# Optimization experiments

Hardware: AMD Instinct MI355X
Metric: run time of the kernel (lower is better)

Reference implementation:

```python
import jax, jax.numpy as jnp
import numpy as np

C0 = 16          # embed channels (c0) == mamba d_model
OUT_DIM = 32
D_INNER = 32     # expand * c0
D_STATE = 16
D_CONV = 4
DT_RANK = 1      # max(1, d_model // 16)
EPS = 1e-5


def setup_inputs():
    key = jax.random.key(0)
    ks = jax.random.split(key, 32)

    def n(i, shape, s):
        return (jax.random.normal(ks[i], shape) * s).astype(jnp.float32)

    inp = {
        "x": jax.random.normal(ks[0], (1, 4, 64, 64, 64), jnp.float32),
        "embed_w": n(1, (4, C0, 1, 7, 7, 7), 0.1),   # 4 per-modality conv7 stems
        "ln_g": jnp.ones((C0,), jnp.float32),
        "ln_b": jnp.zeros((C0,), jnp.float32),
        "in_proj_w": n(2, (2 * D_INNER, C0), 0.25),
        "out_proj_w": n(3, (C0, D_INNER), 0.18),
        "up_w": n(4, (C0, OUT_DIM, 2, 2, 2), 0.2),   # ConvTranspose3d k=2 s=2
    }
    for j, sfx in enumerate(["", "_b"]):             # forward / backward scan params
        b = 5 + 7 * j
        inp["conv_w" + sfx] = n(b, (D_INNER, 1, D_CONV), 0.3)
        inp["conv_b" + sfx] = n(b + 1, (D_INNER,), 0.1)
        inp["xproj_w" + sfx] = n(b + 2, (DT_RANK + 2 * D_STATE, D_INNER), 0.15)
        inp["dtproj_w" + sfx] = n(b + 3, (D_INNER, DT_RANK), 0.5)
        inp["dtproj_b" + sfx] = jnp.full((D_INNER,), -4.6, jnp.float32)  # softplus ~= 0.01
        inp["A_log" + sfx] = jnp.log(jnp.tile(jnp.arange(1, D_STATE + 1, dtype=jnp.float32), (D_INNER, 1)))
        inp["D_skip" + sfx] = jnp.ones((D_INNER,), jnp.float32)
    return inp


def _instnorm(x):
    m = jnp.mean(x, axis=(2, 3, 4), keepdims=True)
    v = jnp.mean(jnp.square(x - m), axis=(2, 3, 4), keepdims=True)
    return (x - m) / jnp.sqrt(v + EPS)


def _embed(x1, w):
    # Conv3d(1, c0, k=7, s=2, p=3, bias=False) -> InstanceNorm3d -> GELU(exact)
    y = jax.lax.conv_general_dilated(x1, w, (2, 2, 2), [(3, 3)] * 3,
                                     dimension_numbers=('NCDHW', 'OIDHW', 'NCDHW'))
    return jax.nn.gelu(_instnorm(y), approximate=False)


def _branch(u, z, cw, cb, xw, dtw, dtb, A_log, D_skip):
    # One Mamba scan branch. u, z: [B, L, Dn]
    Dn = u.shape[-1]
    uc = jax.lax.conv_general_dilated(jnp.swapaxes(u, 1, 2), cw, (1,), [(D_CONV - 1, 0)],
                                      feature_group_count=Dn,
                                      dimension_numbers=('NCH', 'OIH', 'NCH'))
    u = jax.nn.silu(jnp.swapaxes(uc + cb[None, :, None], 1, 2))       # causal dw-conv + SiLU
    xdbl = u @ xw.T                                                   # [B,L,R+2N]
    dt = jax.nn.softplus(xdbl[..., :DT_RANK] @ dtw.T + dtb)           # [B,L,Dn]
    Bm = xdbl[..., DT_RANK:DT_RANK + D_STATE]                         # [B,L,N]
    Cm = xdbl[..., DT_RANK + D_STATE:]                                # [B,L,N]
    A = -jnp.exp(A_log)                                               # [Dn,N]
    a = jnp.exp(dt[..., None] * A)                                    # [B,L,Dn,N]
    b = (dt * u)[..., None] * Bm[:, :, None, :]                       # [B,L,Dn,N]

    def comb(c1, c2):
        a1, b1 = c1
        a2, b2 = c2
        return a1 * a2, a2 * b1 + b2

    _, h = jax.lax.associative_scan(comb, (a, b), axis=1)             # h_t = a_t h_{t-1} + b_t
    y = jnp.einsum('bldn,bln->bld', h, Cm) + u * D_skip
    return y * jax.nn.silu(z)


def _bimamba(t, p):
    xz = t @ p['in_proj_w'].T
    xi, z = jnp.split(xz, 2, axis=-1)
    yf = _branch(xi, z, p['conv_w'], p['conv_b'], p['xproj_w'], p['dtproj_w'],
                 p['dtproj_b'], p['A_log'], p['D_skip'])
    yb = _branch(xi[:, ::-1], z[:, ::-1], p['conv_w_b'], p['conv_b_b'], p['xproj_w_b'],
                 p['dtproj_w_b'], p['dtproj_b_b'], p['A_log_b'], p['D_skip_b'])[:, ::-1]
    return (yf + yb) @ p['out_proj_w'].T


def _mamba_dir(x5, p):
    B, C = x5.shape[:2]
    t = jnp.swapaxes(x5.reshape(B, C, -1), 1, 2)                      # [B, L, C]
    mu = jnp.mean(t, axis=-1, keepdims=True)
    var = jnp.mean(jnp.square(t - mu), axis=-1, keepdims=True)
    t = (t - mu) / jnp.sqrt(var + EPS) * p['ln_g'] + p['ln_b']        # LayerNorm
    t = _bimamba(t, p)
    return jnp.swapaxes(t, 1, 2).reshape(x5.shape)


def _mamba_layer(x5, p):
    # tri-directional scans: (d,w,h), (w,d,h), (h,w,d) + residual
    o1 = _mamba_dir(x5, p)
    o2 = jnp.transpose(_mamba_dir(jnp.transpose(x5, (0, 1, 3, 2, 4)), p), (0, 1, 3, 2, 4))
    o3 = jnp.transpose(_mamba_dir(jnp.transpose(x5, (0, 1, 4, 3, 2)), p), (0, 1, 4, 3, 2))
    return o1 + o2 + o3 + x5


def reference(x, embed_w, ln_g, ln_b, in_proj_w, out_proj_w, up_w,
              conv_w, conv_b, xproj_w, dtproj_w, dtproj_b, A_log, D_skip,
              conv_w_b, conv_b_b, xproj_w_b, dtproj_w_b, dtproj_b_b, A_log_b, D_skip_b):
    p = dict(ln_g=ln_g, ln_b=ln_b, in_proj_w=in_proj_w, out_proj_w=out_proj_w,
             conv_w=conv_w, conv_b=conv_b, xproj_w=xproj_w, dtproj_w=dtproj_w,
             dtproj_b=dtproj_b, A_log=A_log, D_skip=D_skip,
             conv_w_b=conv_w_b, conv_b_b=conv_b_b, xproj_w_b=xproj_w_b,
             dtproj_w_b=dtproj_w_b, dtproj_b_b=dtproj_b_b, A_log_b=A_log_b,
             D_skip_b=D_skip_b)
    us = [_embed(x[:, m:m + 1], embed_w[m]) for m in range(4)]        # 4 modalities
    outs = [_mamba_layer(u, p) for u in us]
    y = outs[0] + outs[1] + outs[2] + outs[3] + us[0] + us[1] + us[2] + us[3]
    B, _, D, H, W = y.shape
    # ConvTranspose3d(c0, out_dim, k=2, s=2): each output 2x2x2 block from one input voxel
    y = jnp.einsum('bcdhw,coijk->bodihjwk', y, up_w).reshape(B, OUT_DIM, 2 * D, 2 * H, 2 * W)
    return y
```

## Files before the change

kernel.cpp:

```cpp
#include <hip/hip_runtime.h>
#include <math.h>

#define L 32768
#define CH 64
#define NC 512

#if __has_builtin(__builtin_amdgcn_exp2f)
#define EXP2(x) __builtin_amdgcn_exp2f(x)
#else
#define EXP2(x) exp2f(x)
#endif

__device__ __forceinline__ int sigma_map(int l, int perm) {
    int b2 = l >> 10, b1 = (l >> 5) & 31, b0 = l & 31;
    if (perm == 0) return (b2 << 10) | (b1 << 5) | b0;
    if (perm == 1) return (b1 << 10) | (b2 << 5) | b0;
    return (b0 << 10) | (b1 << 5) | b2;
}

__device__ __forceinline__ float silu_f(float v) {
    return v / (1.f + __expf(-v));
}
__device__ __forceinline__ float softplus_f(float x) {
    return fmaxf(x, 0.f) + log1pf(__expf(-fabsf(x)));
}

__device__ __forceinline__ float quad_sum(float x) {
    int v = __builtin_amdgcn_update_dpp(0, __float_as_int(x), 0xB1, 0xf, 0xf, true);
    x += __int_as_float(v);
    v = __builtin_amdgcn_update_dpp(0, __float_as_int(x), 0x4E, 0xf, 0xf, true);
    x += __int_as_float(v);
    return x;
}

__global__ __launch_bounds__(256) void k_embed(const float* __restrict__ x,
                                               const float* __restrict__ w,
                                               float* __restrict__ us) {
    __shared__ float tile[10143];
    int bx = blockIdx.x, m = blockIdx.y;
    int c = bx >> 7, sb = bx & 127;
    int zc = sb >> 2, yc0 = (sb & 3) << 3;
    const float* xin = x + m * 262144;
    int iz0 = 2 * zc - 3, iy0 = 2 * yc0 - 3;
    for (int i = threadIdx.x; i < 10143; i += 256) {
        int tz = i / 1449, r = i - tz * 1449;
        int ty = r / 69, tx = r - ty * 69;
        int gz = iz0 + tz, gy = iy0 + ty, gx = tx - 3;
        float v = 0.f;
        if ((unsigned)gz < 64u && (unsigned)gy < 64u && (unsigned)gx < 64u)
            v = xin[(gz * 64 + gy) * 64 + gx];
        tile[i] = v;
    }
    __syncthreads();
    const float* wc = w + (m * 16 + c) * 343;
    int tyl = threadIdx.x >> 5, xc = threadIdx.x & 31;
    float acc = 0.f;
    for (int kz = 0; kz < 7; ++kz)
        for (int ky = 0; ky < 7; ++ky) {
            const float* row = &tile[(kz * 21 + 2 * tyl + ky) * 69 + 2 * xc];
            const float* wr = &wc[kz * 49 + ky * 7];
            #pragma unroll
            for (int kx = 0; kx < 7; ++kx) acc += row[kx] * wr[kx];
        }
    us[(m * 16 + c) * 32768 + sb * 256 + threadIdx.x] = acc;
}

__global__ void k_instnorm_gelu(float* __restrict__ us) {
    int ch = blockIdx.x;
    float* p = us + ch * 32768;
    float s = 0.f, s2 = 0.f;
    for (int i = threadIdx.x; i < 32768; i += 256) { float v = p[i]; s += v; s2 += v * v; }
    __shared__ float rs[256], rs2[256];
    rs[threadIdx.x] = s; rs2[threadIdx.x] = s2;
    __syncthreads();
    for (int o = 128; o > 0; o >>= 1) {
        if (threadIdx.x < o) { rs[threadIdx.x] += rs[threadIdx.x + o]; rs2[threadIdx.x] += rs2[threadIdx.x + o]; }
        __syncthreads();
    }
    float mu = rs[0] * (1.f / 32768.f);
    float var = rs2[0] * (1.f / 32768.f) - mu * mu;
    float rinv = rsqrtf(var + 1e-5f);
    for (int i = threadIdx.x; i < 32768; i += 256) {
        float v = (p[i] - mu) * rinv;
        p[i] = 0.5f * v * (1.f + erff(v * 0.70710678118654752f));
    }
}

__global__ void k_transpose(const float* __restrict__ us, float* __restrict__ us_t) {
    __shared__ float tl[16][257];
    int m = blockIdx.x >> 7, t0 = (blockIdx.x & 127) << 8;
    for (int i = threadIdx.x; i < 4096; i += 256) {
        int c = i >> 8, j = i & 255;
        tl[c][j] = us[(m * 16 + c) * 32768 + t0 + j];
    }
    __syncthreads();
    for (int i = threadIdx.x; i < 4096; i += 256) {
        int j = i >> 4, c = i & 15;
        us_t[(m * 32768 + t0 + j) * 16 + c] = tl[c][j];
    }
}

__global__ __launch_bounds__(512) void k_chunkA(
    const float* __restrict__ us_t, const float* __restrict__ ln_g, const float* __restrict__ ln_b,
    const float* __restrict__ Wip,
    const float* __restrict__ cwA, const float* __restrict__ cbA, const float* __restrict__ xwA,
    const float* __restrict__ dtwA, const float* __restrict__ dtbA, const float* __restrict__ AlA,
    const float* __restrict__ cwB, const float* __restrict__ cbB, const float* __restrict__ xwB,
    const float* __restrict__ dtwB, const float* __restrict__ dtbB, const float* __restrict__ AlB,
    float2* __restrict__ hlPa) {
    __shared__ float sm[8000];
    float* xiT = sm;
    float* uSh = sm + 2304;
    float* sBs = sm + 4480;
    float* xd0 = sm + 5760;
    float* G   = sm + 5824;

    int c = blockIdx.x, dir = blockIdx.y;
    int m = dir / 3, perm = dir - m * 3;
    int p0 = c * CH;
    int tid = threadIdx.x;

    G[tid] = Wip[tid];
    if (tid < 16) G[512 + tid] = ln_g[tid];
    else if (tid < 32) G[512 + tid] = ln_b[tid - 16];
    __syncthreads();

    if (tid < 70) {
        int p = p0 - 3 + tid;
        if ((unsigned)p < (unsigned)L) {
            int sp = sigma_map(p, perm);
            const float4* rw = (const float4*)(us_t + (m * 32768 + sp) * 16);
            float t[16];
            ((float4*)t)[0] = rw[0]; ((float4*)t)[1] = rw[1];
            ((float4*)t)[2] = rw[2]; ((float4*)t)[3] = rw[3];
            float mu = 0.f;
            #pragma unroll
            for (int ci = 0; ci < 16; ++ci) mu += t[ci];
            mu *= (1.f / 16.f);
            float var = 0.f;
            #pragma unroll
            for (int ci = 0; ci < 16; ++ci) { float d = t[ci] - mu; var += d * d; }
            var *= (1.f / 16.f);
            float rinv = rsqrtf(var + 1e-5f);
            #pragma unroll
            for (int ci = 0; ci < 16; ++ci)
                uSh[ci * 72 + tid] = (t[ci] - mu) * rinv * G[512 + ci] + G[528 + ci];
        } else {
            #pragma unroll
            for (int ci = 0; ci < 16; ++ci) uSh[ci * 72 + tid] = 0.f;
        }
    }
    __syncthreads();

    for (int it = tid; it < 576; it += 512) {
        int d = it / 18, q = it - d * 18;
        float ax = 0.f, ay = 0.f, az = 0.f, aw = 0.f;
        #pragma unroll
        for (int ci = 0; ci < 16; ++ci) {
            float4 tq = *(const float4*)&uSh[ci * 72 + 4 * q];
            float wv = G[d * 16 + ci];
            ax += tq.x * wv; ay += tq.y * wv; az += tq.z * wv; aw += tq.w * wv;
        }
        float4 o4 = {ax, ay, az, aw};
        *(float4*)&xiT[d * 72 + 4 * q] = o4;
    }
    __syncthreads();

    for (int b = 0; b < 2; ++b) {
        const float* cw  = b ? cwB  : cwA;
        const float* cb  = b ? cbB  : cbA;
        const float* xw  = b ? xwB  : xwA;
        const float* dtw = b ? dtwB : dtwA;
        const float* dtb = b ? dtbB : dtbA;
        const float* Al  = b ? AlB  : AlA;
        for (int i = tid; i < 544; i += 512) G[i] = xw[i];
        if (tid < 128) G[544 + tid] = cw[tid];
        else if (tid < 160) G[544 + tid] = cb[tid - 128];
        __syncthreads();

        {
            int d = tid >> 4, q = tid & 15, s0 = 4 * q;
            float xr[7];
            if (b == 0) {
                #pragma unroll
                for (int j = 0; j < 7; ++j) xr[j] = xiT[d * 72 + s0 + j];
            } else {
                #pragma unroll
                for (int j = 0; j < 7; ++j) xr[j] = xiT[d * 72 + 63 - s0 + j];
            }
            float w0 = G[544 + d * 4], w1 = G[545 + d * 4], w2 = G[546 + d * 4], w3 = G[547 + d * 4];
            float bias = G[672 + d];
            #pragma unroll
            for (int i = 0; i < 4; ++i) {
                float a;
                if (b == 0) a = bias + xr[i] * w0 + xr[i + 1] * w1 + xr[i + 2] * w2 + xr[i + 3] * w3;
                else        a = bias + xr[6 - i] * w0 + xr[5 - i] * w1 + xr[4 - i] * w2 + xr[3 - i] * w3;
                uSh[d * 68 + s0 + i] = silu_f(a);
            }
        }
        __syncthreads();

        for (int it = tid; it < 272; it += 512) {
            int j = it >> 4, q = it & 15, s0 = 4 * q;
            float ax = 0.f, ay = 0.f, az = 0.f, aw = 0.f;
            #pragma unroll
            for (int ci = 0; ci < 32; ++ci) {
                float4 uq = *(const float4*)&uSh[ci * 68 + s0];
                float wv = G[j * 32 + ci];
                ax += uq.x * wv; ay += uq.y * wv; az += uq.z * wv; aw += uq.w * wv;
            }
            if (j == 0) {
                float4 o4 = {ax, ay, az, aw};
                *(float4*)&xd0[s0] = o4;
            } else {
                sBs[(s0 + 0) * 20 + (j - 1)] = ax;
                sBs[(s0 + 1) * 20 + (j - 1)] = ay;
                sBs[(s0 + 2) * 20 + (j - 1)] = az;
                sBs[(s0 + 3) * 20 + (j - 1)] = aw;
            }
        }
        __syncthreads();

        for (int i = tid; i < 2048; i += 512) {
            int d2 = i >> 6, s = i & 63;
            G[d2 * 68 + s] = softplus_f(xd0[s] * dtw[d2] + dtb[d2]);
        }
        __syncthreads();

        if (tid < 128) {
            int d = tid >> 2, nb = (tid & 3) * 4;
            float kk0 = -1.44269504f * __expf(Al[d * 16 + nb + 0]);
            float kk1 = -1.44269504f * __expf(Al[d * 16 + nb + 1]);
            float kk2 = -1.44269504f * __expf(Al[d * 16 + nb + 2]);
            float kk3 = -1.44269504f * __expf(Al[d * 16 + nb + 3]);
            float h0 = 0.f, h1 = 0.f, h2 = 0.f, h3 = 0.f, sumdt = 0.f;
            const float* dtp = &G[d * 68];
            const float* up  = &uSh[d * 68];
            for (int s0 = 0; s0 < CH; s0 += 4) {
                float4 dt4 = *(const float4*)&dtp[s0];
                float4 u4  = *(const float4*)&up[s0];
                #define ASTEP(DT, UU, SS) { \
                    float w_ = (DT) * (UU); \
                    float4 B4 = *(const float4*)&sBs[(SS) * 20 + nb]; \
                    h0 = fmaf(EXP2((DT) * kk0), h0, w_ * B4.x); \
                    h1 = fmaf(EXP2((DT) * kk1), h1, w_ * B4.y); \
                    h2 = fmaf(EXP2((DT) * kk2), h2, w_ * B4.z); \
                    h3 = fmaf(EXP2((DT) * kk3), h3, w_ * B4.w); \
                    sumdt += (DT); }
                ASTEP(dt4.x, u4.x, s0 + 0)
                ASTEP(dt4.y, u4.y, s0 + 1)
                ASTEP(dt4.z, u4.z, s0 + 2)
                ASTEP(dt4.w, u4.w, s0 + 3)
                #undef ASTEP
            }
            int chunk = b ? (NC - 1 - c) : c;
            float4* o4 = (float4*)(hlPa + (((size_t)(dir * 2 + b) * NC + chunk) * 512) + d * 16 + nb);
            float4 a0 = {h0, EXP2(sumdt * kk0), h1, EXP2(sumdt * kk1)};
            float4 a1 = {h2, EXP2(sumdt * kk2), h3, EXP2(sumdt * kk3)};
            o4[0] = a0; o4[1] = a1;
        }
        __syncthreads();
    }
}

__global__ __launch_bounds__(512) void k_scanB(float2* __restrict__ hlPa) {
    int db = blockIdx.x;
    int t = threadIdx.x;
    float2* base = hlPa + (size_t)db * NC * 512 + t;
    float H = 0.f;
    for (int c0 = 0; c0 < NC; c0 += 8) {
        float2 v[8];
        #pragma unroll
        for (int j = 0; j < 8; ++j) v[j] = base[(c0 + j) * 512];
        #pragma unroll
        for (int j = 0; j < 8; ++j) {
            *((float*)(base + (c0 + j) * 512)) = H;
            H = fmaf(v[j].y, H, v[j].x);
        }
    }
}

__global__ __launch_bounds__(512) void k_chunkC(
    const float* __restrict__ us_t, const float* __restrict__ ln_g, const float* __restrict__ ln_b,
    const float* __restrict__ Wip, const float* __restrict__ Wout,
    const float* __restrict__ cwA, const float* __restrict__ cbA, const float* __restrict__ xwA,
    const float* __restrict__ dtwA, const float* __restrict__ dtbA, const float* __restrict__ AlA,
    const float* __restrict__ DsA,
    const float* __restrict__ cwB, const float* __restrict__ cbB, const float* __restrict__ xwB,
    const float* __restrict__ dtwB, const float* __restrict__ dtbB, const float* __restrict__ AlB,
    const float* __restrict__ DsB,
    const float2* __restrict__ hlPa, float* __restrict__ O) {
    __shared__ float sm[13504];
    float* xiT = sm;
    float* zT  = sm + 2304;
    float* syT = sm + 4608;
    float* uSh = sm + 6784;
    float* sBs = sm + 8960;
    float* sCs = sm + 10240;
    float* xd0 = sm + 11264;
    float* G   = sm + 11328;

    int c = blockIdx.x, dir = blockIdx.y;
    int m = dir / 3, perm = dir - m * 3;
    int p0 = c * CH;
    int tid = threadIdx.x;

    for (int i = tid; i < 1024; i += 512) G[i] = Wip[i];
    if (tid < 16) G[1024 + tid] = ln_g[tid];
    else if (tid < 32) G[1024 + tid] = ln_b[tid - 16];
    __syncthreads();

    if (tid < 70) {
        int p = p0 - 3 + tid;
        if ((unsigned)p < (unsigned)L) {
            int sp = sigma_map(p, perm);
            const float4* rw = (const float4*)(us_t + (m * 32768 + sp) * 16);
            float t[16];
            ((float4*)t)[0] = rw[0]; ((float4*)t)[1] = rw[1];
            ((float4*)t)[2] = rw[2]; ((float4*)t)[3] = rw[3];
            float mu = 0.f;
            #pragma unroll
            for (int ci = 0; ci < 16; ++ci) mu += t[ci];
            mu *= (1.f / 16.f);
            float var = 0.f;
            #pragma unroll
            for (int ci = 0; ci < 16; ++ci) { float d = t[ci] - mu; var += d * d; }
            var *= (1.f / 16.f);
            float rinv = rsqrtf(var + 1e-5f);
            #pragma unroll
            for (int ci = 0; ci < 16; ++ci)
                uSh[ci * 72 + tid] = (t[ci] - mu) * rinv * G[1024 + ci] + G[1040 + ci];
        } else {
            #pragma unroll
            for (int ci = 0; ci < 16; ++ci) uSh[ci * 72 + tid] = 0.f;
        }
    }
    __syncthreads();

    for (int it = tid; it < 1152; it += 512) {
        int dd = it / 18, q = it - dd * 18;
        float ax = 0.f, ay = 0.f, az = 0.f, aw = 0.f;
        #pragma unroll
        for (int ci = 0; ci < 16; ++ci) {
            float4 tq = *(const float4*)&uSh[ci * 72 + 4 * q];
            float wv = G[dd * 16 + ci];
            ax += tq.x * wv; ay += tq.y * wv; az += tq.z * wv; aw += tq.w * wv;
        }
        float4 o4 = {ax, ay, az, aw};
        int d = dd & 31;
        if (dd < 32) *(float4*)&xiT[d * 72 + 4 * q] = o4;
        else         *(float4*)&zT[d * 72 + 4 * q] = o4;
    }
    __syncthreads();

    for (int b = 0; b < 2; ++b) {
        const float* cw  = b ? cwB  : cwA;
        const float* cb  = b ? cbB  : cbA;
        const float* xw  = b ? xwB  : xwA;
        const float* dtw = b ? dtwB : dtwA;
        const float* dtb = b ? dtbB : dtbA;
        const float* Al  = b ? AlB  : AlA;
        const float* Ds  = b ? DsB  : DsA;
        for (int i = tid; i < 1056; i += 512) G[i] = xw[i];
        if (tid < 128) G[1056 + tid] = cw[tid];
        else if (tid < 160) G[1056 + tid] = cb[tid - 128];
        __syncthreads();

        {
            int d = tid >> 4, q = tid & 15, s0 = 4 * q;
            float xr[7];
            if (b == 0) {
                #pragma unroll
                for (int j = 0; j < 7; ++j) xr[j] = xiT[d * 72 + s0 + j];
            } else {
                #pragma unroll
                for (int j = 0; j < 7; ++j) xr[j] = xiT[d * 72 + 63 - s0 + j];
            }
            float w0 = G[1056 + d * 4], w1 = G[1057 + d * 4], w2 = G[1058 + d * 4], w3 = G[1059 + d * 4];
            float bias = G[1184 + d];
            #pragma unroll
            for (int i = 0; i < 4; ++i) {
                float a;
                if (b == 0) a = bias + xr[i] * w0 + xr[i + 1] * w1 + xr[i + 2] * w2 + xr[i + 3] * w3;
                else        a = bias + xr[6 - i] * w0 + xr[5 - i] * w1 + xr[4 - i] * w2 + xr[3 - i] * w3;
                uSh[d * 68 + s0 + i] = silu_f(a);
            }
        }
        __syncthreads();

        for (int it = tid; it < 528; it += 512) {
            int j = it >> 4, q = it & 15, s0 = 4 * q;
            float ax = 0.f, ay = 0.f, az = 0.f, aw = 0.f;
            #pragma unroll
            for (int ci = 0; ci < 32; ++ci) {
                float4 uq = *(const float4*)&uSh[ci * 68 + s0];
                float wv = G[j * 32 + ci];
                ax += uq.x * wv; ay += uq.y * wv; az += uq.z * wv; aw += uq.w * wv;
            }
            if (j == 0) {
                float4 o4 = {ax, ay, az, aw};
                *(float4*)&xd0[s0] = o4;
            } else if (j < 17) {
                sBs[(s0 + 0) * 20 + (j - 1)] = ax;
                sBs[(s0 + 1) * 20 + (j - 1)] = ay;
                sBs[(s0 + 2) * 20 + (j - 1)] = az;
                sBs[(s0 + 3) * 20 + (j - 1)] = aw;
            } else {
                sCs[(s0 + 0) * 16 + (j - 17)] = ax;
                sCs[(s0 + 1) * 16 + (j - 17)] = ay;
                sCs[(s0 + 2) * 16 + (j - 17)] = az;
                sCs[(s0 + 3) * 16 + (j - 17)] = aw;
            }
        }
        __syncthreads();

        for (int i = tid; i < 2048; i += 512) {
            int d2 = i >> 6, s = i & 63;
            G[d2 * 68 + s] = softplus_f(xd0[s] * dtw[d2] + dtb[d2]);
        }
        __syncthreads();

        for (int it = tid; it < 2048; it += 512) {
            int d = it >> 6, s = it & 63;
            float val = uSh[d * 68 + s] * Ds[d];
            if (b == 0) syT[d * 68 + s] = val;
            else        syT[d * 68 + (63 - s)] += val;
        }
        __syncthreads();

        if (tid < 128) {
            int d = tid >> 2, nb = (tid & 3) * 4;
            float kk0 = -1.44269504f * __expf(Al[d * 16 + nb + 0]);
            float kk1 = -1.44269504f * __expf(Al[d * 16 + nb + 1]);
            float kk2 = -1.44269504f * __expf(Al[d * 16 + nb + 2]);
            float kk3 = -1.44269504f * __expf(Al[d * 16 + nb + 3]);
            int chunk = b ? (NC - 1 - c) : c;
            const float2* hp = hlPa + (((size_t)(dir * 2 + b) * NC + chunk) * 512) + d * 16 + nb;
            float h0 = hp[0].x, h1 = hp[1].x, h2 = hp[2].x, h3 = hp[3].x;
            const float* dtp = &G[d * 68];
            const float* up  = &uSh[d * 68];
            for (int s0 = 0; s0 < CH; s0 += 4) {
                float4 dt4 = *(const float4*)&dtp[s0];
                float4 u4  = *(const float4*)&up[s0];
                float pr0, pr1, pr2, pr3;
                #define CSTEP(DT, UU, SS, PR) { \
                    float w_ = (DT) * (UU); \
                    float4 B4 = *(const float4*)&sBs[(SS) * 20 + nb]; \
                    float4 C4 = *(const float4*)&sCs[(SS) * 16 + nb]; \
                    h0 = fmaf(EXP2((DT) * kk0), h0, w_ * B4.x); \
                    h1 = fmaf(EXP2((DT) * kk1), h1, w_ * B4.y); \
                    h2 = fmaf(EXP2((DT) * kk2), h2, w_ * B4.z); \
                    h3 = fmaf(EXP2((DT) * kk3), h3, w_ * B4.w); \
                    float p_ = h0 * C4.x; \
                    p_ = fmaf(h1, C4.y, p_); \
                    p_ = fmaf(h2, C4.z, p_); \
                    p_ = fmaf(h3, C4.w, p_); \
                    PR = quad_sum(p_); }
                CSTEP(dt4.x, u4.x, s0 + 0, pr0)
                CSTEP(dt4.y, u4.y, s0 + 1, pr1)
                CSTEP(dt4.z, u4.z, s0 + 2, pr2)
                CSTEP(dt4.w, u4.w, s0 + 3, pr3)
                #undef CSTEP
                if ((tid & 3) == 0) {
                    if (b == 0) {
                        float4* dst = (float4*)&syT[d * 68 + s0];
                        float4 o = *dst;
                        o.x += pr0; o.y += pr1; o.z += pr2; o.w += pr3;
                        *dst = o;
                    } else {
                        float4* dst = (float4*)&syT[d * 68 + (60 - s0)];
                        float4 o = *dst;
                        o.x += pr3; o.y += pr2; o.z += pr1; o.w += pr0;
                        *dst = o;
                    }
                }
            }
        }
        __syncthreads();
    }

    for (int it = tid; it < 2048; it += 512) {
        int d = it >> 6, pl = it & 63;
        syT[d * 68 + pl] *= silu_f(zT[d * 72 + pl + 3]);
    }
    __syncthreads();

    if (tid < 512) G[tid] = Wout[tid];
    __syncthreads();
    for (int it = tid; it < 1024; it += 512) {
        int p = it >> 4, cc = it & 15;
        float acc = 0.f;
        #pragma unroll
        for (int d = 0; d < 32; ++d) acc += syT[d * 68 + p] * G[cc * 32 + d];
        O[((size_t)(dir * 32768 + p0 + p)) * 16 + cc] = acc;
    }
}

__global__ void k_accum(const float* __restrict__ us_t, const float* __restrict__ O,
                        float* __restrict__ acc_t) {
    int it = blockIdx.x * 256 + threadIdx.x;
    int sp = it >> 2, q = (it & 3) << 2;
    float ax = 0.f, ay = 0.f, az = 0.f, aw = 0.f;
    #pragma unroll
    for (int mm = 0; mm < 4; ++mm) {
        float4 v = *(const float4*)&us_t[(mm * 32768 + sp) * 16 + q];
        ax += 2.f * v.x; ay += 2.f * v.y; az += 2.f * v.z; aw += 2.f * v.w;
    }
    #pragma unroll
    for (int perm = 0; perm < 3; ++perm) {
        int l = sigma_map(sp, perm);
        #pragma unroll
        for (int mm = 0; mm < 4; ++mm) {
            int dir = mm * 3 + perm;
            float4 v = *(const float4*)&O[(dir * 32768 + l) * 16 + q];
            ax += v.x; ay += v.y; az += v.z; aw += v.w;
        }
    }
    float4 o4 = {ax, ay, az, aw};
    *(float4*)&acc_t[sp * 16 + q] = o4;
}

__global__ void k_up(const float* __restrict__ acc_t, const float* __restrict__ upw,
                     float* __restrict__ out) {
    __shared__ float w[4096];
    for (int i = threadIdx.x; i < 4096; i += 256) w[i] = upw[i];
    __syncthreads();
    int e = blockIdx.x * 256 + threadIdx.x;
    int o = e >> 17;
    int r2 = e & 131071;
    int Dz = r2 >> 11, Hy = (r2 >> 5) & 63, Wp = r2 & 31;
    int sp = ((Dz >> 1) << 10) | ((Hy >> 1) << 5) | Wp;
    int wbase = (((Dz & 1) << 2) | ((Hy & 1) << 1));
    const float* arow = &acc_t[sp * 16];
    float v0 = 0.f, v1 = 0.f;
    #pragma unroll
    for (int c = 0; c < 16; ++c) {
        float a = arow[c];
        const float* wr = &w[(c * 32 + o) * 8 + wbase];
        v0 += a * wr[0];
        v1 += a * wr[1];
    }
    float2 ov; ov.x = v0; ov.y = v1;
    *(float2*)&out[((o * 64 + Dz) * 64 + Hy) * 64 + 2 * Wp] = ov;
}

extern "C" void kernel_launch(void* const* d_in, const int* in_sizes, int n_in,
                              void* d_out, int out_size, void* d_ws, size_t ws_size,
                              hipStream_t stream) {
    (void)in_sizes; (void)n_in; (void)out_size; (void)ws_size;
    const float* x    = (const float*)d_in[0];
    const float* embw = (const float*)d_in[1];
    const float* ln_g = (const float*)d_in[2];
    const float* ln_b = (const float*)d_in[3];
    const float* Wip  = (const float*)d_in[4];
    const float* Wout = (const float*)d_in[5];
    const float* upw  = (const float*)d_in[6];
    const float* cwA  = (const float*)d_in[7];
    const float* cbA  = (const float*)d_in[8];
    const float* xwA  = (const float*)d_in[9];
    const float* dtwA = (const float*)d_in[10];
    const float* dtbA = (const float*)d_in[11];
    const float* AlA  = (const float*)d_in[12];
    const float* DsA  = (const float*)d_in[13];
    const float* cwB  = (const float*)d_in[14];
    const float* cbB  = (const float*)d_in[15];
    const float* xwB  = (const float*)d_in[16];
    const float* dtwB = (const float*)d_in[17];
    const float* dtbB = (const float*)d_in[18];
    const float* AlB  = (const float*)d_in[19];
    const float* DsB  = (const float*)d_in[20];

    float* ws    = (float*)d_ws;
    float*  us    = ws;
    float*  us_t  = ws + 2097152;
    float2* hlPa  = (float2*)(ws + 4194304);
    float*  O     = ws + 16777216;
    float*  acc_t = ws + 23068672;

    k_embed<<<dim3(2048, 4), 256, 0, stream>>>(x, embw, us);
    k_instnorm_gelu<<<64, 256, 0, stream>>>(us);
    k_transpose<<<512, 256, 0, stream>>>(us, us_t);
    k_chunkA<<<dim3(NC, 12), 512, 0, stream>>>(us_t, ln_g, ln_b, Wip,
                                               cwA, cbA, xwA, dtwA, dtbA, AlA,
                                               cwB, cbB, xwB, dtwB, dtbB, AlB, hlPa);
    k_scanB<<<24, 512, 0, stream>>>(hlPa);
    k_chunkC<<<dim3(NC, 12), 512, 0, stream>>>(us_t, ln_g, ln_b, Wip, Wout,
                                               cwA, cbA, xwA, dtwA, dtbA, AlA, DsA,
                                               cwB, cbB, xwB, dtwB, dtbB, AlB, DsB,
                                               hlPa, O);
    k_accum<<<512, 256, 0, stream>>>(us_t, O, acc_t);
    k_up<<<16384, 256, 0, stream>>>(acc_t, upw, (float*)d_out);
}
```

Baseline: 928.7 us.

## Spread selective-scan states across more threads in chunk kernels

In the chunk-summary kernel, each of the 512 threads now scans a single (channel, state) pair instead of 128 threads each handling four states. The B projection is stored transposed as [state][step] so each thread reads it as contiguous float4. In the output kernel, 256 threads each carry two states instead of 128 threads carrying four, and the C-dot reduction grows from a 4-lane to an 8-lane DPP sum. The goal is a shorter serial dependency chain per thread and more parallel work during the scan, at the cost of more exp evaluations per step and an extra cross-lane reduction step.

```diff
diff --git a/kernel.cpp b/kernel.cpp
--- a/kernel.cpp
+++ b/kernel.cpp
@@ -25,10 +25,12 @@
     return fmaxf(x, 0.f) + log1pf(__expf(-fabsf(x)));
 }
 
-__device__ __forceinline__ float quad_sum(float x) {
+__device__ __forceinline__ float oct_sum(float x) {
     int v = __builtin_amdgcn_update_dpp(0, __float_as_int(x), 0xB1, 0xf, 0xf, true);
     x += __int_as_float(v);
     v = __builtin_amdgcn_update_dpp(0, __float_as_int(x), 0x4E, 0xf, 0xf, true);
+    x += __int_as_float(v);
+    v = __builtin_amdgcn_update_dpp(0, __float_as_int(x), 0x124, 0xf, 0xf, true);
     x += __int_as_float(v);
     return x;
 }
@@ -108,12 +110,12 @@
     const float* __restrict__ cwB, const float* __restrict__ cbB, const float* __restrict__ xwB,
     const float* __restrict__ dtwB, const float* __restrict__ dtbB, const float* __restrict__ AlB,
     float2* __restrict__ hlPa) {
-    __shared__ float sm[8000];
+    __shared__ float sm[7808];
     float* xiT = sm;
     float* uSh = sm + 2304;
-    float* sBs = sm + 4480;
-    float* xd0 = sm + 5760;
-    float* G   = sm + 5824;
+    float* sB  = sm + 4480;
+    float* xd0 = sm + 5568;
+    float* G   = sm + 5632;
 
     int c = blockIdx.x, dir = blockIdx.y;
     int m = dir / 3, perm = dir - m * 3;
@@ -209,15 +211,9 @@
                 float wv = G[j * 32 + ci];
                 ax += uq.x * wv; ay += uq.y * wv; az += uq.z * wv; aw += uq.w * wv;
             }
-            if (j == 0) {
-                float4 o4 = {ax, ay, az, aw};
-                *(float4*)&xd0[s0] = o4;
-            } else {
-                sBs[(s0 + 0) * 20 + (j - 1)] = ax;
-                sBs[(s0 + 1) * 20 + (j - 1)] = ay;
-                sBs[(s0 + 2) * 20 + (j - 1)] = az;
-                sBs[(s0 + 3) * 20 + (j - 1)] = aw;
-            }
+            float4 o4 = {ax, ay, az, aw};
+            if (j == 0) *(float4*)&xd0[s0] = o4;
+            else        *(float4*)&sB[(j - 1) * 68 + s0] = o4;
         }
         __syncthreads();
 
@@ -227,37 +223,26 @@
         }
         __syncthreads();
 
-        if (tid < 128) {
-            int d = tid >> 2, nb = (tid & 3) * 4;
-            float kk0 = -1.44269504f * __expf(Al[d * 16 + nb + 0]);
-            float kk1 = -1.44269504f * __expf(Al[d * 16 + nb + 1]);
-            float kk2 = -1.44269504f * __expf(Al[d * 16 + nb + 2]);
-            float kk3 = -1.44269504f * __expf(Al[d * 16 + nb + 3]);
-            float h0 = 0.f, h1 = 0.f, h2 = 0.f, h3 = 0.f, sumdt = 0.f;
+        {
+            int d = tid >> 4, n = tid & 15;
+            float A = -__expf(Al[tid]);
+            float h = 0.f, sumdt = 0.f;
             const float* dtp = &G[d * 68];
             const float* up  = &uSh[d * 68];
+            const float* Bp  = &sB[n * 68];
             for (int s0 = 0; s0 < CH; s0 += 4) {
                 float4 dt4 = *(const float4*)&dtp[s0];
                 float4 u4  = *(const float4*)&up[s0];
-                #define ASTEP(DT, UU, SS) { \
-                    float w_ = (DT) * (UU); \
-                    float4 B4 = *(const float4*)&sBs[(SS) * 20 + nb]; \
-                    h0 = fmaf(EXP2((DT) * kk0), h0, w_ * B4.x); \
-                    h1 = fmaf(EXP2((DT) * kk1), h1, w_ * B4.y); \
-                    h2 = fmaf(EXP2((DT) * kk2), h2, w_ * B4.z); \
-                    h3 = fmaf(EXP2((DT) * kk3), h3, w_ * B4.w); \
-                    sumdt += (DT); }
-                ASTEP(dt4.x, u4.x, s0 + 0)
-                ASTEP(dt4.y, u4.y, s0 + 1)
-                ASTEP(dt4.z, u4.z, s0 + 2)
-                ASTEP(dt4.w, u4.w, s0 + 3)
-                #undef ASTEP
+                float4 B4  = *(const float4*)&Bp[s0];
+                h = fmaf(__expf(dt4.x * A), h, dt4.x * u4.x * B4.x);
+                h = fmaf(__expf(dt4.y * A), h, dt4.y * u4.y * B4.y);
+                h = fmaf(__expf(dt4.z * A), h, dt4.z * u4.z * B4.z);
+                h = fmaf(__expf(dt4.w * A), h, dt4.w * u4.w * B4.w);
+                sumdt += (dt4.x + dt4.y) + (dt4.z + dt4.w);
             }
             int chunk = b ? (NC - 1 - c) : c;
-            float4* o4 = (float4*)(hlPa + (((size_t)(dir * 2 + b) * NC + chunk) * 512) + d * 16 + nb);
-            float4 a0 = {h0, EXP2(sumdt * kk0), h1, EXP2(sumdt * kk1)};
-            float4 a1 = {h2, EXP2(sumdt * kk2), h3, EXP2(sumdt * kk3)};
-            o4[0] = a0; o4[1] = a1;
+            float2 v; v.x = h; v.y = __expf(sumdt * A);
+            hlPa[(((size_t)(dir * 2 + b) * NC + chunk) * 512) + tid] = v;
         }
         __syncthreads();
     }
@@ -428,15 +413,13 @@
         }
         __syncthreads();
 
-        if (tid < 128) {
-            int d = tid >> 2, nb = (tid & 3) * 4;
+        if (tid < 256) {
+            int d = tid >> 3, nb = (tid & 7) * 2;
             float kk0 = -1.44269504f * __expf(Al[d * 16 + nb + 0]);
             float kk1 = -1.44269504f * __expf(Al[d * 16 + nb + 1]);
-            float kk2 = -1.44269504f * __expf(Al[d * 16 + nb + 2]);
-            float kk3 = -1.44269504f * __expf(Al[d * 16 + nb + 3]);
             int chunk = b ? (NC - 1 - c) : c;
             const float2* hp = hlPa + (((size_t)(dir * 2 + b) * NC + chunk) * 512) + d * 16 + nb;
-            float h0 = hp[0].x, h1 = hp[1].x, h2 = hp[2].x, h3 = hp[3].x;
+            float h0 = hp[0].x, h1 = hp[1].x;
             const float* dtp = &G[d * 68];
             const float* up  = &uSh[d * 68];
             for (int s0 = 0; s0 < CH; s0 += 4) {
@@ -445,23 +428,18 @@
                 float pr0, pr1, pr2, pr3;
                 #define CSTEP(DT, UU, SS, PR) { \
                     float w_ = (DT) * (UU); \
-                    float4 B4 = *(const float4*)&sBs[(SS) * 20 + nb]; \
-                    float4 C4 = *(const float4*)&sCs[(SS) * 16 + nb]; \
-                    h0 = fmaf(EXP2((DT) * kk0), h0, w_ * B4.x); \
-                    h1 = fmaf(EXP2((DT) * kk1), h1, w_ * B4.y); \
-                    h2 = fmaf(EXP2((DT) * kk2), h2, w_ * B4.z); \
-                    h3 = fmaf(EXP2((DT) * kk3), h3, w_ * B4.w); \
-                    float p_ = h0 * C4.x; \
-                    p_ = fmaf(h1, C4.y, p_); \
-                    p_ = fmaf(h2, C4.z, p_); \
-                    p_ = fmaf(h3, C4.w, p_); \
-                    PR = quad_sum(p_); }
+                    float2 B2 = *(const float2*)&sBs[(SS) * 20 + nb]; \
+                    float2 C2 = *(const float2*)&sCs[(SS) * 16 + nb]; \
+                    h0 = fmaf(EXP2((DT) * kk0), h0, w_ * B2.x); \
+                    h1 = fmaf(EXP2((DT) * kk1), h1, w_ * B2.y); \
+                    float p_ = fmaf(h1, C2.y, h0 * C2.x); \
+                    PR = oct_sum(p_); }
                 CSTEP(dt4.x, u4.x, s0 + 0, pr0)
                 CSTEP(dt4.y, u4.y, s0 + 1, pr1)
                 CSTEP(dt4.z, u4.z, s0 + 2, pr2)
                 CSTEP(dt4.w, u4.w, s0 + 3, pr3)
                 #undef CSTEP
-                if ((tid & 3) == 0) {
+                if ((tid & 7) == 0) {
                     if (b == 0) {
                         float4* dst = (float4*)&syT[d * 68 + s0];
                         float4 o = *dst;
```

After: 862.5 us. 1.08x faster.
